# Performance work log

Measured on AMD Instinct MI355X. Metric: run time of the kernel, lower is better.

## Reference

```python
import jax, jax.numpy as jnp
import numpy as np

B = 4096        # graphs per batch
N_PER = 64      # nodes per graph
N = B * N_PER   # total nodes
D = 512         # embed_dim
T = 2048        # target_size


def setup_inputs() -> dict:
    key = jax.random.key(0)
    k1, k2, k3 = jax.random.split(key, 3)
    batch_emb = jax.random.normal(k1, (N, D), dtype=jnp.float32)
    # sorted per-node graph ids (PyG `batch` vector), all graphs non-empty
    seg = jnp.repeat(jnp.arange(B, dtype=jnp.int64), N_PER)
    # local node indices of the two query nodes in each graph
    targets = jax.random.randint(k2, (B, 2), 0, N_PER, dtype=jnp.int64)
    W = jax.random.normal(k3, (T, 3 * D), dtype=jnp.float32) * (1.0 / np.sqrt(3 * D))
    b = jnp.zeros((T,), dtype=jnp.float32)
    return {"batch_emb": batch_emb, "seg": seg, "targets": targets, "W": W, "b": b}


def reference(batch_emb, seg, targets, W, b):
    # per-graph mean pooling (segment mean)
    sums = jax.ops.segment_sum(batch_emb, seg, num_segments=B)          # [B, D]
    counts = jax.ops.segment_sum(jnp.ones((batch_emb.shape[0],), batch_emb.dtype),
                                 seg, num_segments=B)                   # [B]
    node_avg = sums / counts[:, None]                                   # [B, D]
    # convert local query indices to global node indices via segment starts
    starts = jnp.cumsum(counts.astype(jnp.int64)) - counts.astype(jnp.int64)  # [B]
    global_idx = starts[:, None] + targets                              # [B, 2]
    q = batch_emb[global_idx]                                           # [B, 2, D]
    final_embs = jnp.concatenate([q[:, 0], q[:, 1], node_avg], axis=-1) # [B, 3D]
    return final_embs @ W.T + b                                         # [B, T]
```

## Files before the change

kernel.cpp:

```cpp
#include <hip/hip_runtime.h>
#include <hip/hip_bf16.h>
#include <stdint.h>

#define B_GRAPHS 4096
#define N_PER    64
#define D_EMB    512
#define T_OUT    2048
#define K_DIM    1536
#define WCONV_BLOCKS 512

#define BM   128
#define BN   256
#define BK   32
#define KT_N (K_DIM/BK)
#define NBUF 3

typedef __bf16 bf16x8 __attribute__((ext_vector_type(8)));
typedef float  f32x4  __attribute__((ext_vector_type(4)));

__global__ __launch_bounds__(128) void pool_conv_kernel(
    const float* __restrict__ emb, const int* __restrict__ targets,
    const float* __restrict__ W,
    __hip_bfloat16* __restrict__ lhs, __hip_bfloat16* __restrict__ wb)
{
    union Pack { __hip_bfloat16 h[4]; uint2 u; };

    if (blockIdx.x >= B_GRAPHS) {
        const int total = T_OUT * K_DIM / 4;
        const int nthr  = WCONV_BLOCKS * 128;
        for (int i = (blockIdx.x - B_GRAPHS) * 128 + threadIdx.x;
             i < total; i += nthr) {
            const float4 v = reinterpret_cast<const float4*>(W)[i];
            Pack p;
            p.h[0] = __float2bfloat16(v.x); p.h[1] = __float2bfloat16(v.y);
            p.h[2] = __float2bfloat16(v.z); p.h[3] = __float2bfloat16(v.w);
            reinterpret_cast<uint2*>(wb)[i] = p.u;
        }
        return;
    }

    const int g = blockIdx.x;
    const int t = threadIdx.x;
    const int t0 = targets[2*g];
    const int t1 = targets[2*g + 1];
    const float4* rows = reinterpret_cast<const float4*>(emb)
                         + (size_t)g * N_PER * (D_EMB/4) + t;
    float4 acc = make_float4(0.f, 0.f, 0.f, 0.f);
    #pragma unroll 16
    for (int n = 0; n < N_PER; ++n) {
        float4 v = rows[(size_t)n * (D_EMB/4)];
        acc.x += v.x; acc.y += v.y; acc.z += v.z; acc.w += v.w;
    }
    const float s = 1.0f / (float)N_PER;
    float4 avg = make_float4(acc.x*s, acc.y*s, acc.z*s, acc.w*s);
    float4 q0 = rows[(size_t)t0 * (D_EMB/4)];
    float4 q1 = rows[(size_t)t1 * (D_EMB/4)];

    __hip_bfloat16* row = lhs + (size_t)g * K_DIM;
    Pack p0, p1, pa;
    p0.h[0] = __float2bfloat16(q0.x); p0.h[1] = __float2bfloat16(q0.y);
    p0.h[2] = __float2bfloat16(q0.z); p0.h[3] = __float2bfloat16(q0.w);
    p1.h[0] = __float2bfloat16(q1.x); p1.h[1] = __float2bfloat16(q1.y);
    p1.h[2] = __float2bfloat16(q1.z); p1.h[3] = __float2bfloat16(q1.w);
    pa.h[0] = __float2bfloat16(avg.x); pa.h[1] = __float2bfloat16(avg.y);
    pa.h[2] = __float2bfloat16(avg.z); pa.h[3] = __float2bfloat16(avg.w);
    reinterpret_cast<uint2*>(row)[t]             = p0.u;
    reinterpret_cast<uint2*>(row + D_EMB)[t]     = p1.u;
    reinterpret_cast<uint2*>(row + 2*D_EMB)[t]   = pa.u;
}

__global__ __launch_bounds__(256, 2) void gemm_kernel(
    const __hip_bfloat16* __restrict__ A,
    const __hip_bfloat16* __restrict__ Bm,
    const float* __restrict__ bias,
    float* __restrict__ C)
{
    __shared__ __align__(16) __hip_bfloat16 As[NBUF][BM*BK];
    __shared__ __align__(16) __hip_bfloat16 Bs[NBUF][BN*BK];

    const int t  = threadIdx.x;
    const int w  = t >> 6;
    const int l  = t & 63;
    const int wr = w >> 1;
    const int wc = w & 1;
    const int brow = blockIdx.y * BM;
    const int bcol = blockIdx.x * BN;

    const int srow = l >> 2;
    const int scol = (l & 3) * 8;

    f32x4 acc[4][8];
    #pragma unroll
    for (int m = 0; m < 4; ++m)
        #pragma unroll
        for (int n = 0; n < 8; ++n)
            acc[m][n] = (f32x4){0.f, 0.f, 0.f, 0.f};

    auto stage = [&](int b, int kt) {
        const int k0 = kt * BK;
        char* Ab = reinterpret_cast<char*>(As[b]);
        char* Bb = reinterpret_cast<char*>(Bs[b]);
        #pragma unroll
        for (int c = 0; c < 2; ++c) {
            const int ch = w * 2 + c;
            const __hip_bfloat16* ga =
                A + (size_t)(brow + ch*16 + srow) * K_DIM + k0 + scol;
            __builtin_amdgcn_global_load_lds(
                (const __attribute__((address_space(1))) void*)ga,
                (__attribute__((address_space(3))) void*)(Ab + ch*1024), 16, 0, 0);
        }
        #pragma unroll
        for (int c = 0; c < 4; ++c) {
            const int ch = w * 4 + c;
            const __hip_bfloat16* gb =
                Bm + (size_t)(bcol + ch*16 + srow) * K_DIM + k0 + scol;
            __builtin_amdgcn_global_load_lds(
                (const __attribute__((address_space(1))) void*)gb,
                (__attribute__((address_space(3))) void*)(Bb + ch*1024), 16, 0, 0);
        }
    };

    stage(0, 0);
    stage(1, 1);

    const int kb = (l >> 4) * 16;

    for (int kt = 0; kt < KT_N; ++kt) {
        if (kt + 1 < KT_N) asm volatile("s_waitcnt vmcnt(6)" ::: "memory");
        else               asm volatile("s_waitcnt vmcnt(0)" ::: "memory");
        __builtin_amdgcn_s_barrier();

        if (kt + 2 < KT_N) stage((kt + 2) % NBUF, kt + 2);

        const char* Ab = reinterpret_cast<const char*>(As[kt % NBUF]);
        const char* Bb = reinterpret_cast<const char*>(Bs[kt % NBUF]);

        bf16x8 af[4], bf[8];
        #pragma unroll
        for (int m = 0; m < 4; ++m) {
            const int r = wr*64 + m*16 + (l & 15);
            af[m] = *reinterpret_cast<const bf16x8*>(Ab + r*64 + kb);
        }
        #pragma unroll
        for (int n = 0; n < 8; ++n) {
            const int r = wc*128 + n*16 + (l & 15);
            bf[n] = *reinterpret_cast<const bf16x8*>(Bb + r*64 + kb);
        }
        #pragma unroll
        for (int m = 0; m < 4; ++m)
            #pragma unroll
            for (int n = 0; n < 8; ++n)
                acc[m][n] = __builtin_amdgcn_mfma_f32_16x16x32_bf16(
                                af[m], bf[n], acc[m][n], 0, 0, 0);
    }

    #pragma unroll
    for (int n = 0; n < 8; ++n) {
        const int col = bcol + wc*128 + n*16 + (l & 15);
        const float bv = bias[col];
        #pragma unroll
        for (int m = 0; m < 4; ++m) {
            const int row0 = brow + wr*64 + m*16 + (l >> 4)*4;
            #pragma unroll
            for (int e = 0; e < 4; ++e) {
                __builtin_nontemporal_store(acc[m][n][e] + bv,
                    &C[(size_t)(row0 + e) * T_OUT + col]);
            }
        }
    }
}

extern "C" void kernel_launch(void* const* d_in, const int* in_sizes, int n_in,
                              void* d_out, int out_size, void* d_ws, size_t ws_size,
                              hipStream_t stream) {
    const float* emb     = (const float*)d_in[0];
    const int*   targets = (const int*)d_in[2];
    const float* W       = (const float*)d_in[3];
    const float* bias    = (const float*)d_in[4];
    float* out = (float*)d_out;

    __hip_bfloat16* lhs = (__hip_bfloat16*)d_ws;
    __hip_bfloat16* wb  = lhs + (size_t)B_GRAPHS * K_DIM;

    pool_conv_kernel<<<B_GRAPHS + WCONV_BLOCKS, 128, 0, stream>>>(
        emb, targets, W, lhs, wb);
    gemm_kernel<<<dim3(T_OUT/BN, B_GRAPHS/BM), 256, 0, stream>>>(lhs, wb, bias, out);
}
```

Before: 175.9 us.

## Shrink GEMM N-tile to 128 and remap LDS layout to fragment order

Reduces the GEMM block tile from 128x256 to 128x128, halving per-wave accumulators and doubling the grid. It also changes the global-to-LDS load mapping so each 16-row chunk is stored directly in MFMA fragment order, which makes LDS reads contiguous per lane. Global pointers are now incremented instead of recomputed, and the prefetch of stage kt+2 is issued after the fragment reads instead of before them. The smaller tile lowers register pressure and may raise occupancy, but it reduces operand reuse per block and increases total global and L2 traffic for A.

```diff
diff --git a/kernel.cpp b/kernel.cpp
--- a/kernel.cpp
+++ b/kernel.cpp
@@ -10,7 +10,7 @@
 #define WCONV_BLOCKS 512
 
 #define BM   128
-#define BN   256
+#define BN   128
 #define BK   32
 #define KT_N (K_DIM/BK)
 #define NBUF 3
@@ -86,77 +86,72 @@
     const int brow = blockIdx.y * BM;
     const int bcol = blockIdx.x * BN;
 
-    const int srow = l >> 2;
-    const int scol = (l & 3) * 8;
+    const size_t lane_off = (size_t)(l & 15) * K_DIM + (size_t)(l >> 4) * 8;
 
-    f32x4 acc[4][8];
+    const __hip_bfloat16* pA0 = A  + (size_t)(brow + (2*w    )*16) * K_DIM + lane_off;
+    const __hip_bfloat16* pA1 = A  + (size_t)(brow + (2*w + 1)*16) * K_DIM + lane_off;
+    const __hip_bfloat16* pB0 = Bm + (size_t)(bcol + (2*w    )*16) * K_DIM + lane_off;
+    const __hip_bfloat16* pB1 = Bm + (size_t)(bcol + (2*w + 1)*16) * K_DIM + lane_off;
+
+    f32x4 acc[4][4];
     #pragma unroll
     for (int m = 0; m < 4; ++m)
         #pragma unroll
-        for (int n = 0; n < 8; ++n)
+        for (int n = 0; n < 4; ++n)
             acc[m][n] = (f32x4){0.f, 0.f, 0.f, 0.f};
 
-    auto stage = [&](int b, int kt) {
-        const int k0 = kt * BK;
+    auto stage = [&](int b) {
         char* Ab = reinterpret_cast<char*>(As[b]);
         char* Bb = reinterpret_cast<char*>(Bs[b]);
-        #pragma unroll
-        for (int c = 0; c < 2; ++c) {
-            const int ch = w * 2 + c;
-            const __hip_bfloat16* ga =
-                A + (size_t)(brow + ch*16 + srow) * K_DIM + k0 + scol;
-            __builtin_amdgcn_global_load_lds(
-                (const __attribute__((address_space(1))) void*)ga,
-                (__attribute__((address_space(3))) void*)(Ab + ch*1024), 16, 0, 0);
-        }
-        #pragma unroll
-        for (int c = 0; c < 4; ++c) {
-            const int ch = w * 4 + c;
-            const __hip_bfloat16* gb =
-                Bm + (size_t)(bcol + ch*16 + srow) * K_DIM + k0 + scol;
-            __builtin_amdgcn_global_load_lds(
-                (const __attribute__((address_space(1))) void*)gb,
-                (__attribute__((address_space(3))) void*)(Bb + ch*1024), 16, 0, 0);
-        }
+        __builtin_amdgcn_global_load_lds(
+            (const __attribute__((address_space(1))) void*)pA0,
+            (__attribute__((address_space(3))) void*)(Ab + (2*w    )*1024), 16, 0, 0);
+        __builtin_amdgcn_global_load_lds(
+            (const __attribute__((address_space(1))) void*)pA1,
+            (__attribute__((address_space(3))) void*)(Ab + (2*w + 1)*1024), 16, 0, 0);
+        __builtin_amdgcn_global_load_lds(
+            (const __attribute__((address_space(1))) void*)pB0,
+            (__attribute__((address_space(3))) void*)(Bb + (2*w    )*1024), 16, 0, 0);
+        __builtin_amdgcn_global_load_lds(
+            (const __attribute__((address_space(1))) void*)pB1,
+            (__attribute__((address_space(3))) void*)(Bb + (2*w + 1)*1024), 16, 0, 0);
+        pA0 += BK; pA1 += BK; pB0 += BK; pB1 += BK;
     };
 
-    stage(0, 0);
-    stage(1, 1);
+    stage(0);
+    stage(1);
 
-    const int kb = (l >> 4) * 16;
-
+    int cur = 0;
     for (int kt = 0; kt < KT_N; ++kt) {
-        if (kt + 1 < KT_N) asm volatile("s_waitcnt vmcnt(6)" ::: "memory");
+        if (kt + 1 < KT_N) asm volatile("s_waitcnt vmcnt(4)" ::: "memory");
         else               asm volatile("s_waitcnt vmcnt(0)" ::: "memory");
         __builtin_amdgcn_s_barrier();
 
-        if (kt + 2 < KT_N) stage((kt + 2) % NBUF, kt + 2);
+        const char* Ab = reinterpret_cast<const char*>(As[cur]);
+        const char* Bb = reinterpret_cast<const char*>(Bs[cur]);
+        bf16x8 af[4], bf[4];
+        #pragma unroll
+        for (int m = 0; m < 4; ++m)
+            af[m] = *reinterpret_cast<const bf16x8*>(Ab + (wr*4 + m)*1024 + l*16);
+        #pragma unroll
+        for (int n = 0; n < 4; ++n)
+            bf[n] = *reinterpret_cast<const bf16x8*>(Bb + (wc*4 + n)*1024 + l*16);
 
-        const char* Ab = reinterpret_cast<const char*>(As[kt % NBUF]);
-        const char* Bb = reinterpret_cast<const char*>(Bs[kt % NBUF]);
+        if (kt + 2 < KT_N) stage(cur == 0 ? 2 : cur - 1);
 
-        bf16x8 af[4], bf[8];
-        #pragma unroll
-        for (int m = 0; m < 4; ++m) {
-            const int r = wr*64 + m*16 + (l & 15);
-            af[m] = *reinterpret_cast<const bf16x8*>(Ab + r*64 + kb);
-        }
-        #pragma unroll
-        for (int n = 0; n < 8; ++n) {
-            const int r = wc*128 + n*16 + (l & 15);
-            bf[n] = *reinterpret_cast<const bf16x8*>(Bb + r*64 + kb);
-        }
         #pragma unroll
         for (int m = 0; m < 4; ++m)
             #pragma unroll
-            for (int n = 0; n < 8; ++n)
+            for (int n = 0; n < 4; ++n)
                 acc[m][n] = __builtin_amdgcn_mfma_f32_16x16x32_bf16(
                                 af[m], bf[n], acc[m][n], 0, 0, 0);
+
+        cur = (cur == 2) ? 0 : cur + 1;
     }
 
     #pragma unroll
-    for (int n = 0; n < 8; ++n) {
-        const int col = bcol + wc*128 + n*16 + (l & 15);
+    for (int n = 0; n < 4; ++n) {
+        const int col = bcol + wc*64 + n*16 + (l & 15);
         const float bv = bias[col];
         #pragma unroll
         for (int m = 0; m < 4; ++m) {
```

New measurement: 161.5 us. -8.2%, faster.
